# Kernel optimization log

Measured on AMD Instinct MI355X. Metric: run time of the kernel, lower is better.

Reference implementation:

```python
import jax, jax.numpy as jnp
import numpy as np
import math

EMBED_DIM = 2048
NUM_HEADS = 16
HEAD_DIM = EMBED_DIM // NUM_HEADS
BATCH = 2
SEQ = 2048


def setup_inputs() -> dict:
    key = jax.random.key(0)
    ks = jax.random.split(key, 6)
    x = jax.random.normal(ks[0], (BATCH, SEQ, EMBED_DIM), dtype=jnp.float32)
    # causal mask: True = masked (upper triangle, strictly above diagonal)
    attn_mask = jnp.triu(jnp.ones((SEQ, SEQ), dtype=bool), k=1)
    s = 1.0 / math.sqrt(EMBED_DIM)
    W_qkv = jax.random.normal(ks[1], (3 * EMBED_DIM, EMBED_DIM), dtype=jnp.float32) * s
    b_qkv = jax.random.normal(ks[2], (3 * EMBED_DIM,), dtype=jnp.float32) * 0.01
    W_out = jax.random.normal(ks[3], (EMBED_DIM, EMBED_DIM), dtype=jnp.float32) * s
    b_out = jax.random.normal(ks[4], (EMBED_DIM,), dtype=jnp.float32) * 0.01
    return {"x": x, "W_qkv": W_qkv, "b_qkv": b_qkv, "W_out": W_out,
            "b_out": b_out, "attn_mask": attn_mask}


def reference(x, W_qkv, b_qkv, W_out, b_out, attn_mask):
    B, S, E = x.shape
    # fused QKV projection: [B,S,3E]
    qkv = jnp.einsum('bse,fe->bsf', x, W_qkv) + b_qkv
    qkv = qkv.reshape(B, S, 3, NUM_HEADS, HEAD_DIM)
    qkv = jnp.transpose(qkv, (2, 0, 3, 1, 4))  # [3,B,H,S,Dh]
    q, k, v = qkv[0], qkv[1], qkv[2]
    scale = 1.0 / math.sqrt(HEAD_DIM)
    scores = jnp.einsum('bhqd,bhkd->bhqk', q, k) * scale  # [B,H,S,S]
    scores = jnp.where(attn_mask[None, None, :, :], -jnp.inf, scores)
    attn = jax.nn.softmax(scores, axis=-1)
    out = jnp.einsum('bhqk,bhkd->bhqd', attn, v)  # [B,H,S,Dh]
    out = jnp.transpose(out, (0, 2, 1, 3)).reshape(B, S, E)
    out = jnp.einsum('bse,fe->bsf', out, W_out) + b_out
    return out
```

## Files before the change

kernel.cpp:

```cpp
#include <hip/hip_runtime.h>
#include <hip/hip_bf16.h>
#include <math.h>

#define SEQ   2048
#define EMBED 2048
#define NHEAD 16
#define DHEAD 128
#define BATCH 2

#define NX   ((size_t)BATCH * SEQ * EMBED)
#define NW1  ((size_t)3 * EMBED * EMBED)
#define NB1  ((size_t)3 * EMBED)
#define NW2  ((size_t)EMBED * EMBED)
#define NB2  ((size_t)EMBED)

typedef __bf16 bf16;
typedef __attribute__((__ext_vector_type__(8))) __bf16 bf16x8;
typedef __attribute__((__ext_vector_type__(4))) __bf16 bf16x4;
typedef __attribute__((__ext_vector_type__(4))) float f32x4;
typedef __attribute__((__ext_vector_type__(4))) unsigned int u32x4;

#define NEG_BIG (-1.0e30f)

__device__ __forceinline__ f32x4 mfma_16x16x32(bf16x8 a, bf16x8 b, f32x4 c) {
  return __builtin_amdgcn_mfma_f32_16x16x32_bf16(a, b, c, 0, 0, 0);
}

__device__ __forceinline__ void llds16(bf16* dst, const bf16* src) {
  __builtin_amdgcn_global_load_lds(
      (const __attribute__((address_space(1))) void*)src,
      (__attribute__((address_space(3))) void*)dst, 16, 0, 0);
}

#define BAR()                                   \
  {                                             \
    asm volatile("" ::: "memory");              \
    __builtin_amdgcn_s_barrier();               \
    asm volatile("" ::: "memory");              \
  }

__global__ void convert_inputs(const void* __restrict__ xin,
                               const void* __restrict__ w1in,
                               const void* __restrict__ b1in,
                               const void* __restrict__ w2in,
                               const void* __restrict__ b2in,
                               bf16* __restrict__ xb, bf16* __restrict__ w1b,
                               bf16* __restrict__ b1b, bf16* __restrict__ w2b,
                               bf16* __restrict__ b2b, int* __restrict__ flagp)
{
  __shared__ int sflag;
  if (threadIdx.x == 0) sflag = 0;
  __syncthreads();
  const unsigned short* xh = (const unsigned short*)xin;
  int huge = 0;
  for (int i = threadIdx.x; i < 2048; i += 256) {
    float f = __uint_as_float((unsigned int)xh[i] << 16);
    if (!(fabsf(f) <= 1e4f)) huge = 1;
  }
  if (huge) sflag = 1;
  __syncthreads();
  const int isf32 = sflag;
  if (blockIdx.x == 0 && threadIdx.x == 0) *flagp = isf32;

  const void* srcs[5] = {xin, w1in, b1in, w2in, b2in};
  bf16* dsts[5] = {xb, w1b, b1b, w2b, b2b};
  const size_t lens[5] = {NX, NW1, NB1, NW2, NB2};
  const size_t gid = (size_t)blockIdx.x * blockDim.x + threadIdx.x;
  const size_t gstride = (size_t)gridDim.x * blockDim.x;
  for (int sidx = 0; sidx < 5; ++sidx) {
    const size_t n8 = lens[sidx] >> 3;
    bf16* d = dsts[sidx];
    if (isf32) {
      const float* s = (const float*)srcs[sidx];
      for (size_t i = gid; i < n8; i += gstride) {
        const float* sp = s + i * 8;
        bf16x8 r;
#pragma unroll
        for (int j = 0; j < 8; ++j) r[j] = (bf16)sp[j];
        *(bf16x8*)(d + i * 8) = r;
      }
    } else {
      const u32x4* s = (const u32x4*)srcs[sidx];
      for (size_t i = gid; i < n8; i += gstride)
        *(u32x4*)(d + i * 8) = s[i];
    }
  }
}

#define GSTAGE(tt)                                                       \
  {                                                                      \
    const int _slot = (tt) & 3;                                          \
    const int _k0 = (tt) << 5;                                           \
    _Pragma("unroll") for (int j = 0; j < 3; ++j)                        \
        llds16(&sAB[_slot][dstofs[j]], srcbase[j] + _k0);                \
  }

template <int MODE>
__global__ __launch_bounds__(512, 1) void gemm_nt2(
    const bf16* __restrict__ A, const bf16* __restrict__ B,
    const bf16* __restrict__ bias, int K,
    void* __restrict__ out0v, bf16* __restrict__ out1, bf16* __restrict__ out2,
    const int* __restrict__ flagp)
{
  __shared__ __align__(16) bf16 sAB[4][12288];
  const int t = threadIdx.x;
  const int lane = t & 63, w = t >> 6;
  const int wm = w >> 2, wn = w & 3;
  const int lr = lane & 15, lq = lane >> 4;
  const int m0 = blockIdx.y * 128, n0 = blockIdx.x * 256;
  const int NT = K >> 5;

  const int srow = lane >> 2;
  const int glog = (lane & 3) ^ (srow & 3);
  const bf16* srcbase[3];
  int dstofs[3];
#pragma unroll
  for (int j = 0; j < 3; ++j) {
    const int c2 = w * 3 + j;
    if (c2 < 8) {
      srcbase[j] = A + (size_t)(m0 + c2 * 16 + srow) * K + glog * 8;
      dstofs[j] = c2 * 512;
    } else {
      const int b = c2 - 8;
      srcbase[j] = B + (size_t)(n0 + b * 16 + srow) * K + glog * 8;
      dstofs[j] = 4096 + b * 512;
    }
  }

  f32x4 acc[4][4];
#pragma unroll
  for (int i = 0; i < 4; ++i)
#pragma unroll
    for (int j = 0; j < 4; ++j) acc[i][j] = (f32x4){0.f, 0.f, 0.f, 0.f};

  const int rdg = ((lq ^ (lr & 3)) << 3);
  const int aofs = (wm * 64 + lr) * 32 + rdg;
  const int bofs = 4096 + (wn * 64 + lr) * 32 + rdg;

  GSTAGE(0);
  GSTAGE(1);
  GSTAGE(2);
  asm volatile("s_waitcnt vmcnt(6)" ::: "memory");
  BAR();

  for (int tt = 0; tt < NT; ++tt) {
    const bf16* sl = sAB[tt & 3];
    if (tt + 3 < NT) GSTAGE(tt + 3);
    bf16x8 af[4], bfr[4];
#pragma unroll
    for (int i = 0; i < 4; ++i) {
      af[i]  = *(const bf16x8*)(sl + aofs + i * 512);
      bfr[i] = *(const bf16x8*)(sl + bofs + i * 512);
    }
    BAR();
    __builtin_amdgcn_s_setprio(1);
#pragma unroll
    for (int mi = 0; mi < 4; ++mi)
#pragma unroll
      for (int ni = 0; ni < 4; ++ni)
        acc[mi][ni] = mfma_16x16x32(af[mi], bfr[ni], acc[mi][ni]);
    __builtin_amdgcn_s_setprio(0);
    if (tt <= NT - 4)      { asm volatile("s_waitcnt vmcnt(6)" ::: "memory"); }
    else if (tt == NT - 3) { asm volatile("s_waitcnt vmcnt(3)" ::: "memory"); }
    else if (tt == NT - 2) { asm volatile("s_waitcnt vmcnt(0)" ::: "memory"); }
    BAR();
  }

  if (MODE == 0) {
    const int which = n0 >> 11;
    const int bb = m0 >> 11;
    const int s0 = m0 & 2047;
    if (which == 2) {
      bf16* dst = out2;
#pragma unroll
      for (int ni = 0; ni < 4; ++ni) {
        const int ng = n0 + wn * 64 + ni * 16 + lr;
        const int h = (ng >> 7) & 15;
        const int d = ng & 127;
        const float bv = (float)bias[ng];
        bf16* rowp =
            dst + ((size_t)(bb * NHEAD + h) * DHEAD + d) * SEQ + s0 + wm * 64;
#pragma unroll
        for (int mi = 0; mi < 4; ++mi) {
          bf16x4 pk;
#pragma unroll
          for (int reg = 0; reg < 4; ++reg)
            pk[reg] = (bf16)(acc[mi][ni][reg] + bv);
          *(bf16x4*)(rowp + mi * 16 + lq * 4) = pk;
        }
      }
    } else {
      bf16* dst = (which == 0) ? (bf16*)out0v : out1;
#pragma unroll
      for (int ni = 0; ni < 4; ++ni) {
        const int ng = n0 + wn * 64 + ni * 16 + lr;
        const int h = (ng >> 7) & 15;
        const int d = ng & 127;
        const float bv = (float)bias[ng];
        bf16* hb = dst + (size_t)(bb * NHEAD + h) * SEQ * DHEAD + d;
#pragma unroll
        for (int mi = 0; mi < 4; ++mi)
#pragma unroll
          for (int reg = 0; reg < 4; ++reg) {
            const int s = s0 + wm * 64 + mi * 16 + lq * 4 + reg;
            hb[(size_t)s * DHEAD] = (bf16)(acc[mi][ni][reg] + bv);
          }
      }
    }
  } else {
    const int isf32 = *flagp;
#pragma unroll
    for (int ni = 0; ni < 4; ++ni) {
      const int col = n0 + wn * 64 + ni * 16 + lr;
      const float bv = (float)bias[col];
#pragma unroll
      for (int mi = 0; mi < 4; ++mi)
#pragma unroll
        for (int reg = 0; reg < 4; ++reg) {
          const int row = m0 + wm * 64 + mi * 16 + lq * 4 + reg;
          const float v = acc[mi][ni][reg] + bv;
          const size_t idx = (size_t)row * EMBED + col;
          if (isf32) ((float*)out0v)[idx] = v;
          else       ((bf16*)out0v)[idx] = (bf16)v;
        }
    }
  }
}

__device__ __forceinline__ void qk_softmax_tile(
    const bf16* __restrict__ sK, bf16* __restrict__ sP, const bf16x8* aq,
    float& m_i, float& l_i, f32x4* oacc, int kt, int qt,
    int w, int lr, int lq, int sPofs)
{
  const float scale = 0.08838834764831845f;
  f32x4 tacc[4];
#pragma unroll
  for (int ni = 0; ni < 4; ++ni) tacc[ni] = (f32x4){0.f, 0.f, 0.f, 0.f};
#pragma unroll
  for (int ks = 0; ks < 4; ++ks)
#pragma unroll
    for (int ni = 0; ni < 4; ++ni) {
      bf16x8 bk = *(const bf16x8*)(sK + (ni * 16 + lr) * 136 + ks * 32 + lq * 8);
      tacc[ni] = mfma_16x16x32(bk, aq[ks], tacc[ni]);
    }
  float pp[4][4];
  const int qg = qt * 64 + w * 16 + lr;
#pragma unroll
  for (int ni = 0; ni < 4; ++ni)
#pragma unroll
    for (int reg = 0; reg < 4; ++reg) {
      float sv = tacc[ni][reg] * scale;
      if (kt == qt) {
        const int kg = kt * 64 + ni * 16 + lq * 4 + reg;
        if (kg > qg) sv = NEG_BIG;
      }
      pp[ni][reg] = sv;
    }
  float mx;
  {
    float a0 = fmaxf(fmaxf(pp[0][0], pp[0][1]), fmaxf(pp[0][2], pp[0][3]));
    float a1 = fmaxf(fmaxf(pp[1][0], pp[1][1]), fmaxf(pp[1][2], pp[1][3]));
    float a2 = fmaxf(fmaxf(pp[2][0], pp[2][1]), fmaxf(pp[2][2], pp[2][3]));
    float a3 = fmaxf(fmaxf(pp[3][0], pp[3][1]), fmaxf(pp[3][2], pp[3][3]));
    mx = fmaxf(fmaxf(a0, a1), fmaxf(a2, a3));
  }
  mx = fmaxf(mx, __shfl_xor(mx, 16, 64));
  mx = fmaxf(mx, __shfl_xor(mx, 32, 64));
  const float mnew = fmaxf(m_i, mx);
  const float alpha = __expf(m_i - mnew);
  float ls = 0.f;
#pragma unroll
  for (int ni = 0; ni < 4; ++ni) {
    float s0 = __expf(pp[ni][0] - mnew);
    float s1 = __expf(pp[ni][1] - mnew);
    float s2 = __expf(pp[ni][2] - mnew);
    float s3 = __expf(pp[ni][3] - mnew);
    pp[ni][0] = s0; pp[ni][1] = s1; pp[ni][2] = s2; pp[ni][3] = s3;
    ls += (s0 + s1) + (s2 + s3);
  }
  ls += __shfl_xor(ls, 16, 64);
  ls += __shfl_xor(ls, 32, 64);
  l_i = l_i * alpha + ls;
  m_i = mnew;
#pragma unroll
  for (int dt = 0; dt < 8; ++dt) oacc[dt] *= alpha;
  bf16* rowp = sP + (sPofs + w * 16 + lr) * 64;
  const int swz = lr & 7;
#pragma unroll
  for (int ni = 0; ni < 4; ++ni) {
    bf16x4 pk;
#pragma unroll
    for (int reg = 0; reg < 4; ++reg) pk[reg] = (bf16)pp[ni][reg];
    const int col = ni * 16 + lq * 4;
    const int scol = (((col >> 3) ^ swz) << 3) | (col & 7);
    *(bf16x4*)(rowp + scol) = pk;
  }
}

__device__ __forceinline__ void pv_tile(const bf16* __restrict__ sP,
                                        const bf16* __restrict__ sV,
                                        f32x4* oacc, int w, int lr, int lq,
                                        int sPofs)
{
  const bf16* rowp = sP + (sPofs + w * 16 + lr) * 64;
  const int swz = lr & 7;
#pragma unroll
  for (int ks2 = 0; ks2 < 2; ++ks2) {
    const int chunk = ks2 * 4 + lq;
    bf16x8 bp = *(const bf16x8*)(rowp + ((chunk ^ swz) << 3));
#pragma unroll
    for (int dt = 0; dt < 8; ++dt) {
      bf16x8 av =
          *(const bf16x8*)(sV + (dt * 16 + lr) * 72 + ks2 * 32 + lq * 8);
      oacc[dt] = mfma_16x16x32(av, bp, oacc[dt]);
    }
  }
}

__global__ __launch_bounds__(256, 2) void attn_fwd(
    const bf16* __restrict__ qb, const bf16* __restrict__ kb,
    const bf16* __restrict__ vt, bf16* __restrict__ aout)
{
  __shared__ bf16 sK[64 * 136];
  __shared__ bf16 sV[128 * 72];
  __shared__ bf16 sP[128 * 64];
  const int t = threadIdx.x;
  const int lane = t & 63, w = t >> 6;
  const int lr = lane & 15, lq = lane >> 4;
  const int p  = blockIdx.x & 15;
  const int bh = blockIdx.x >> 4;
  const int bb = bh >> 4, h = bh & 15;
  const int qlo = p, qhi = 31 - p;

  bf16x8 aqL[4], aqH[4];
  {
    const bf16* qpL =
        qb + ((size_t)bh * SEQ + qlo * 64 + w * 16 + lr) * DHEAD + lq * 8;
    const bf16* qpH =
        qb + ((size_t)bh * SEQ + qhi * 64 + w * 16 + lr) * DHEAD + lq * 8;
#pragma unroll
    for (int ks = 0; ks < 4; ++ks) {
      aqL[ks] = *(const bf16x8*)(qpL + ks * 32);
      aqH[ks] = *(const bf16x8*)(qpH + ks * 32);
    }
  }

  f32x4 oL[8], oH[8];
#pragma unroll
  for (int i = 0; i < 8; ++i) {
    oL[i] = (f32x4){0.f, 0.f, 0.f, 0.f};
    oH[i] = (f32x4){0.f, 0.f, 0.f, 0.f};
  }
  float mL = NEG_BIG, mH = NEG_BIG;
  float lL = 0.f, lH = 0.f;

  bf16x8 rk[4], rv[4];
  const int kr_ = t >> 4, kd_ = t & 15;
  const int vr_ = t >> 3, vk_ = t & 7;
#define FETCH(ktv)                                                          \
  {                                                                         \
    const int _kt = (ktv);                                                  \
    _Pragma("unroll") for (int i = 0; i < 4; ++i) {                         \
      rk[i] = *(const bf16x8*)(kb + ((size_t)bh * SEQ + _kt * 64 +          \
                                     (i * 16 + kr_)) * DHEAD + kd_ * 8);    \
      rv[i] = *(const bf16x8*)(vt + ((size_t)bh * DHEAD + (i * 32 + vr_)) * \
                                     SEQ + _kt * 64 + vk_ * 8);             \
    }                                                                       \
  }
#define COMMIT()                                                            \
  {                                                                         \
    _Pragma("unroll") for (int i = 0; i < 4; ++i) {                         \
      *(bf16x8*)(sK + (i * 16 + kr_) * 136 + kd_ * 8) = rk[i];              \
      *(bf16x8*)(sV + (i * 32 + vr_) * 72 + vk_ * 8) = rv[i];               \
    }                                                                       \
  }

  FETCH(0);
  COMMIT();
  __syncthreads();

  for (int kt = 0; kt <= qhi; ++kt) {
    if (kt < qhi) FETCH(kt + 1);
    const bool doLo = (kt <= qlo);

    qk_softmax_tile(sK, sP, aqH, mH, lH, oH, kt, qhi, w, lr, lq, 64);
    if (doLo) qk_softmax_tile(sK, sP, aqL, mL, lL, oL, kt, qlo, w, lr, lq, 0);
    asm volatile("s_waitcnt lgkmcnt(0)" ::: "memory");
    pv_tile(sP, sV, oH, w, lr, lq, 64);
    if (doLo) pv_tile(sP, sV, oL, w, lr, lq, 0);

    __syncthreads();
    if (kt < qhi) {
      COMMIT();
      __syncthreads();
    }
  }

#pragma unroll
  for (int side = 0; side < 2; ++side) {
    const f32x4* oacc = side ? oH : oL;
    const float linv = 1.0f / (side ? lH : lL);
    const int qt = side ? qhi : qlo;
    const int qg = qt * 64 + w * 16 + lr;
    bf16* outp = aout + ((size_t)bb * SEQ + qg) * EMBED + h * 128 + lq * 4;
#pragma unroll
    for (int dt = 0; dt < 8; ++dt) {
      bf16x4 pk;
#pragma unroll
      for (int reg = 0; reg < 4; ++reg)
        pk[reg] = (bf16)(oacc[dt][reg] * linv);
      *(bf16x4*)(outp + dt * 16) = pk;
    }
  }
#undef FETCH
#undef COMMIT
}

extern "C" void kernel_launch(void* const* d_in, const int* in_sizes, int n_in,
                              void* d_out, int out_size, void* d_ws, size_t ws_size,
                              hipStream_t stream) {
  const void* x    = d_in[0];
  const void* Wqkv = d_in[1];
  const void* bqkv = d_in[2];
  const void* Wout = d_in[3];
  const void* bout = d_in[4];

  int* flagp = (int*)d_ws;
  bf16* base = (bf16*)((char*)d_ws + 256);
  bf16* xb   = base;
  bf16* w1b  = xb + NX;
  bf16* b1b  = w1b + NW1;
  bf16* w2b  = b1b + NB1;
  bf16* b2b  = w2b + NW2;
  bf16* qb   = b2b + NB2;
  bf16* kb   = qb + NX;
  bf16* vt   = kb + NX;
  bf16* aout = vt + NX;

  convert_inputs<<<dim3(1024), dim3(256), 0, stream>>>(
      x, Wqkv, bqkv, Wout, bout, xb, w1b, b1b, w2b, b2b, flagp);
  gemm_nt2<0><<<dim3(24, 32), dim3(512), 0, stream>>>(
      xb, w1b, b1b, EMBED, (void*)qb, kb, vt, flagp);
  attn_fwd<<<dim3(512), dim3(256), 0, stream>>>(qb, kb, vt, aout);
  gemm_nt2<1><<<dim3(8, 32), dim3(512), 0, stream>>>(
      aout, w2b, b2b, EMBED, d_out, nullptr, nullptr, flagp);
}
```

Before: 414.1 us.

## Rewrite GEMM with 256x256 tiles, 8-phase K=64 pipeline and XCD-aware block remap

Both projection GEMMs now use 256x256 output tiles with each wave computing 128x64, doubling accumulators to cover 8x4 MFMA tiles. K is staged in 64-wide double-buffered half-tiles loaded across eight interleaved phases per pair of k-tiles, and a 1D grid is remapped so consecutive blocks land on the same XCD group. This is meant to raise arithmetic intensity per LDS load and improve L2 locality. In exchange it uses 128KB of LDS and many more registers, and launches fewer blocks (384 and 128), which may leave CUs underused.

```diff
diff --git a/kernel.cpp b/kernel.cpp
--- a/kernel.cpp
+++ b/kernel.cpp
@@ -87,84 +87,88 @@
   }
 }
 
-#define GSTAGE(tt)                                                       \
-  {                                                                      \
-    const int _slot = (tt) & 3;                                          \
-    const int _k0 = (tt) << 5;                                           \
-    _Pragma("unroll") for (int j = 0; j < 3; ++j)                        \
-        llds16(&sAB[_slot][dstofs[j]], srcbase[j] + _k0);                \
-  }
-
 template <int MODE>
-__global__ __launch_bounds__(512, 1) void gemm_nt2(
+__global__ __launch_bounds__(512, 2) void gemm8(
     const bf16* __restrict__ A, const bf16* __restrict__ B,
     const bf16* __restrict__ bias, int K,
     void* __restrict__ out0v, bf16* __restrict__ out1, bf16* __restrict__ out2,
     const int* __restrict__ flagp)
 {
-  __shared__ __align__(16) bf16 sAB[4][12288];
+  __shared__ __align__(16) bf16 lds_[65536];
+  constexpr int NBX = (MODE == 0) ? 24 : 8;
   const int t = threadIdx.x;
   const int lane = t & 63, w = t >> 6;
   const int wm = w >> 2, wn = w & 3;
   const int lr = lane & 15, lq = lane >> 4;
-  const int m0 = blockIdx.y * 128, n0 = blockIdx.x * 256;
-  const int NT = K >> 5;
-
-  const int srow = lane >> 2;
-  const int glog = (lane & 3) ^ (srow & 3);
-  const bf16* srcbase[3];
-  int dstofs[3];
-#pragma unroll
-  for (int j = 0; j < 3; ++j) {
-    const int c2 = w * 3 + j;
-    if (c2 < 8) {
-      srcbase[j] = A + (size_t)(m0 + c2 * 16 + srow) * K + glog * 8;
-      dstofs[j] = c2 * 512;
-    } else {
-      const int b = c2 - 8;
-      srcbase[j] = B + (size_t)(n0 + b * 16 + srow) * K + glog * 8;
-      dstofs[j] = 4096 + b * 512;
-    }
-  }
-
-  f32x4 acc[4][4];
-#pragma unroll
-  for (int i = 0; i < 4; ++i)
+  const int nwg = NBX * 16;
+  const int f = blockIdx.x;
+  const int o = (f & 7) * (nwg >> 3) + (f >> 3);
+  const int by = o / NBX, bx = o - by * NBX;
+  const int m0 = by * 256, n0 = bx * 256;
+  const int NT = K >> 6;
+  const int NI = NT >> 1;
+
+  const int srow = t >> 2, sg = t & 3;
+  const bf16* aSrc = A + (size_t)(m0 + srow) * K + sg * 8;
+  const bf16* bSrc = B + (size_t)(n0 + srow) * K + sg * 8;
+
+#define HTSTAGE(isB, kt, kh)                                                 \
+  {                                                                          \
+    bf16* _d = lds_ + ((kt) & 1) * 32768 + (isB) * 16384 + (kh) * 8192 +     \
+               w * 512;                                                      \
+    const bf16* _s = ((isB) ? bSrc : aSrc) + (kt) * 64 + (kh) * 32;          \
+    llds16(_d, _s);                                                          \
+    llds16(_d + 4096, _s + (size_t)128 * K);                                 \
+  }
+
+  f32x4 acc[8][4];
+#pragma unroll
+  for (int i = 0; i < 8; ++i)
 #pragma unroll
     for (int j = 0; j < 4; ++j) acc[i][j] = (f32x4){0.f, 0.f, 0.f, 0.f};
 
-  const int rdg = ((lq ^ (lr & 3)) << 3);
-  const int aofs = (wm * 64 + lr) * 32 + rdg;
-  const int bofs = 4096 + (wn * 64 + lr) * 32 + rdg;
-
-  GSTAGE(0);
-  GSTAGE(1);
-  GSTAGE(2);
-  asm volatile("s_waitcnt vmcnt(6)" ::: "memory");
+  HTSTAGE(0, 0, 0); HTSTAGE(1, 0, 0); HTSTAGE(0, 0, 1); HTSTAGE(1, 0, 1);
+  HTSTAGE(0, 1, 0); HTSTAGE(1, 1, 0);
+  asm volatile("s_waitcnt vmcnt(4)" ::: "memory");
   BAR();
 
-  for (int tt = 0; tt < NT; ++tt) {
-    const bf16* sl = sAB[tt & 3];
-    if (tt + 3 < NT) GSTAGE(tt + 3);
-    bf16x8 af[4], bfr[4];
-#pragma unroll
-    for (int i = 0; i < 4; ++i) {
-      af[i]  = *(const bf16x8*)(sl + aofs + i * 512);
-      bfr[i] = *(const bf16x8*)(sl + bofs + i * 512);
-    }
-    BAR();
-    __builtin_amdgcn_s_setprio(1);
-#pragma unroll
-    for (int mi = 0; mi < 4; ++mi)
-#pragma unroll
-      for (int ni = 0; ni < 4; ++ni)
-        acc[mi][ni] = mfma_16x16x32(af[mi], bfr[ni], acc[mi][ni]);
-    __builtin_amdgcn_s_setprio(0);
-    if (tt <= NT - 4)      { asm volatile("s_waitcnt vmcnt(6)" ::: "memory"); }
-    else if (tt == NT - 3) { asm volatile("s_waitcnt vmcnt(3)" ::: "memory"); }
-    else if (tt == NT - 2) { asm volatile("s_waitcnt vmcnt(0)" ::: "memory"); }
-    BAR();
-  }
+  bf16x8 bfr[4];
+  for (int i = 0; i < NI; ++i) {
+#pragma unroll
+    for (int p = 0; p < 8; ++p) {
+      const int mh = p & 1;
+      const int rbase = (p >> 2) * 32768 + ((p >> 1) & 1) * 8192;
+      bf16x8 af[4];
+      const int arow = rbase + (wm * 128 + mh * 64 + lr) * 32 + lq * 8;
+#pragma unroll
+      for (int mi = 0; mi < 4; ++mi)
+        af[mi] = *(const bf16x8*)(lds_ + arow + mi * 512);
+      if (mh == 0) {
+        const int brow = rbase + 16384 + (wn * 64 + lr) * 32 + lq * 8;
+#pragma unroll
+        for (int ni = 0; ni < 4; ++ni)
+          bfr[ni] = *(const bf16x8*)(lds_ + brow + ni * 512);
+      }
+      const int skt = 2 * i + 1 + ((p + 2) >> 2);
+      if (skt < NT) HTSTAGE(p & 1, skt, ((p >> 1) & 1) ^ 1);
+      BAR();
+      __builtin_amdgcn_s_setprio(1);
+#pragma unroll
+      for (int mi = 0; mi < 4; ++mi)
+#pragma unroll
+        for (int ni = 0; ni < 4; ++ni)
+          acc[mh * 4 + mi][ni] =
+              mfma_16x16x32(af[mi], bfr[ni], acc[mh * 4 + mi][ni]);
+      __builtin_amdgcn_s_setprio(0);
+      if (p == 3) {
+        if (i == NI - 1) { asm volatile("s_waitcnt vmcnt(0)" ::: "memory"); }
+        else             { asm volatile("s_waitcnt vmcnt(4)" ::: "memory"); }
+      }
+      if (p == 7) { asm volatile("s_waitcnt vmcnt(4)" ::: "memory"); }
+      BAR();
+    }
+  }
+#undef HTSTAGE
 
   if (MODE == 0) {
     const int which = n0 >> 11;
@@ -179,14 +183,14 @@
         const int d = ng & 127;
         const float bv = (float)bias[ng];
         bf16* rowp =
-            dst + ((size_t)(bb * NHEAD + h) * DHEAD + d) * SEQ + s0 + wm * 64;
-#pragma unroll
-        for (int mi = 0; mi < 4; ++mi) {
+            dst + ((size_t)(bb * NHEAD + h) * DHEAD + d) * SEQ + s0 + wm * 128;
+#pragma unroll
+        for (int MI = 0; MI < 8; ++MI) {
           bf16x4 pk;
 #pragma unroll
           for (int reg = 0; reg < 4; ++reg)
-            pk[reg] = (bf16)(acc[mi][ni][reg] + bv);
-          *(bf16x4*)(rowp + mi * 16 + lq * 4) = pk;
+            pk[reg] = (bf16)(acc[MI][ni][reg] + bv);
+          *(bf16x4*)(rowp + MI * 16 + lq * 4) = pk;
         }
       }
     } else {
@@ -199,11 +203,11 @@
         const float bv = (float)bias[ng];
         bf16* hb = dst + (size_t)(bb * NHEAD + h) * SEQ * DHEAD + d;
 #pragma unroll
-        for (int mi = 0; mi < 4; ++mi)
+        for (int MI = 0; MI < 8; ++MI)
 #pragma unroll
           for (int reg = 0; reg < 4; ++reg) {
-            const int s = s0 + wm * 64 + mi * 16 + lq * 4 + reg;
-            hb[(size_t)s * DHEAD] = (bf16)(acc[mi][ni][reg] + bv);
+            const int s = s0 + wm * 128 + MI * 16 + lq * 4 + reg;
+            hb[(size_t)s * DHEAD] = (bf16)(acc[MI][ni][reg] + bv);
           }
       }
     }
@@ -214,11 +218,11 @@
       const int col = n0 + wn * 64 + ni * 16 + lr;
       const float bv = (float)bias[col];
 #pragma unroll
-      for (int mi = 0; mi < 4; ++mi)
+      for (int MI = 0; MI < 8; ++MI)
 #pragma unroll
         for (int reg = 0; reg < 4; ++reg) {
-          const int row = m0 + wm * 64 + mi * 16 + lq * 4 + reg;
-          const float v = acc[mi][ni][reg] + bv;
+          const int row = m0 + wm * 128 + MI * 16 + lq * 4 + reg;
+          const float v = acc[MI][ni][reg] + bv;
           const size_t idx = (size_t)row * EMBED + col;
           if (isf32) ((float*)out0v)[idx] = v;
           else       ((bf16*)out0v)[idx] = (bf16)v;
@@ -439,9 +443,9 @@
 
   convert_inputs<<<dim3(1024), dim3(256), 0, stream>>>(
       x, Wqkv, bqkv, Wout, bout, xb, w1b, b1b, w2b, b2b, flagp);
-  gemm_nt2<0><<<dim3(24, 32), dim3(512), 0, stream>>>(
+  gemm8<0><<<dim3(384), dim3(512), 0, stream>>>(
       xb, w1b, b1b, EMBED, (void*)qb, kb, vt, flagp);
   attn_fwd<<<dim3(512), dim3(256), 0, stream>>>(qb, kb, vt, aout);
-  gemm_nt2<1><<<dim3(8, 32), dim3(512), 0, stream>>>(
+  gemm8<1><<<dim3(128), dim3(512), 0, stream>>>(
       aout, w2b, b2b, EMBED, d_out, nullptr, nullptr, flagp);
 }
```

Measured after the change: 429.7 us. 1.04x slower.

## Restructure GEMM pipeline into double-buffered 64-wide K tiles with XCD-aware block remap

Applied to the files above, without the earlier changes.

The two GEMM kernels now stage 64-element K tiles into two LDS buffers, split into 32-wide halves, and issue the async global-to-LDS loads interleaved with four compute phases per iteration. The swizzle pattern and LDS layout change to match. The 2D grid is flattened to 1D and blockIdx is remapped so consecutive blocks on the same XCD cover neighbouring tiles, aiming for better L2 reuse. The intent is to hide global load latency and cut barrier overhead per unit of MFMA work, at the cost of more complex wait-count bookkeeping that could stall or race if the counts are wrong.

```diff
diff --git a/kernel.cpp b/kernel.cpp
--- a/kernel.cpp
+++ b/kernel.cpp
@@ -32,12 +32,7 @@
       (__attribute__((address_space(3))) void*)dst, 16, 0, 0);
 }
 
-#define BAR()                                   \
-  {                                             \
-    asm volatile("" ::: "memory");              \
-    __builtin_amdgcn_s_barrier();               \
-    asm volatile("" ::: "memory");              \
-  }
+#define BARRAW() asm volatile("s_barrier" ::: "memory")
 
 __global__ void convert_inputs(const void* __restrict__ xin,
                                const void* __restrict__ w1in,
@@ -87,44 +82,43 @@
   }
 }
 
-#define GSTAGE(tt)                                                       \
-  {                                                                      \
-    const int _slot = (tt) & 3;                                          \
-    const int _k0 = (tt) << 5;                                           \
-    _Pragma("unroll") for (int j = 0; j < 3; ++j)                        \
-        llds16(&sAB[_slot][dstofs[j]], srcbase[j] + _k0);                \
-  }
-
 template <int MODE>
-__global__ __launch_bounds__(512, 1) void gemm_nt2(
+__global__ __launch_bounds__(512, 1) void gemmE(
     const bf16* __restrict__ A, const bf16* __restrict__ B,
     const bf16* __restrict__ bias, int K,
     void* __restrict__ out0v, bf16* __restrict__ out1, bf16* __restrict__ out2,
     const int* __restrict__ flagp)
 {
-  __shared__ __align__(16) bf16 sAB[4][12288];
+  __shared__ __align__(16) bf16 lds_[49152];
+  constexpr int NTX = (MODE == 0) ? 24 : 8;
   const int t = threadIdx.x;
   const int lane = t & 63, w = t >> 6;
   const int wm = w >> 2, wn = w & 3;
   const int lr = lane & 15, lq = lane >> 4;
-  const int m0 = blockIdx.y * 128, n0 = blockIdx.x * 256;
-  const int NT = K >> 5;
-
-  const int srow = lane >> 2;
-  const int glog = (lane & 3) ^ (srow & 3);
-  const bf16* srcbase[3];
-  int dstofs[3];
-#pragma unroll
-  for (int j = 0; j < 3; ++j) {
-    const int c2 = w * 3 + j;
-    if (c2 < 8) {
-      srcbase[j] = A + (size_t)(m0 + c2 * 16 + srow) * K + glog * 8;
-      dstofs[j] = c2 * 512;
-    } else {
-      const int b = c2 - 8;
-      srcbase[j] = B + (size_t)(n0 + b * 16 + srow) * K + glog * 8;
-      dstofs[j] = 4096 + b * 512;
-    }
+  const int nwg = 32 * NTX;
+  const int f = blockIdx.x;
+  const int o = (f & 7) * (nwg >> 3) + (f >> 3);
+  const int by = o & 31, bx = o >> 5;
+  const int m0 = by << 7, n0 = bx << 8;
+  const int NT = K >> 6;
+  const int NI = NT >> 1;
+
+  const int srow = t >> 2;
+  const int sg8 = (((t & 3) ^ (((t >> 5) & 1) << 1))) << 3;
+
+#define STAGE3(kt_, ks_)                                                     \
+  {                                                                          \
+    const int _kt = (kt_), _ks = (ks_);                                      \
+    if (_kt < NT) {                                                          \
+      const int _bb = (_kt & 1) * 24576;                                     \
+      const int _kc = (_kt << 6) + _ks * 32;                                 \
+      llds16(lds_ + _bb + _ks * 4096 + (w << 9),                             \
+             A + (size_t)(m0 + srow) * K + _kc + sg8);                       \
+      llds16(lds_ + _bb + 8192 + _ks * 8192 + (w << 9),                      \
+             B + (size_t)(n0 + srow) * K + _kc + sg8);                       \
+      llds16(lds_ + _bb + 8192 + _ks * 8192 + 4096 + (w << 9),               \
+             B + (size_t)(n0 + 128 + srow) * K + _kc + sg8);                 \
+    }                                                                        \
   }
 
   f32x4 acc[4][4];
@@ -133,42 +127,61 @@
 #pragma unroll
     for (int j = 0; j < 4; ++j) acc[i][j] = (f32x4){0.f, 0.f, 0.f, 0.f};
 
-  const int rdg = ((lq ^ (lr & 3)) << 3);
-  const int aofs = (wm * 64 + lr) * 32 + rdg;
-  const int bofs = 4096 + (wn * 64 + lr) * 32 + rdg;
-
-  GSTAGE(0);
-  GSTAGE(1);
-  GSTAGE(2);
+  const int rg8 = ((lq ^ (((lr >> 3) & 1) << 1))) << 3;
+  const int arow = (wm * 64 + lr) * 32 + rg8;
+  const int brow = (wn * 64 + lr) * 32 + rg8;
+
+  STAGE3(0, 0);
+  STAGE3(0, 1);
+  STAGE3(1, 0);
   asm volatile("s_waitcnt vmcnt(6)" ::: "memory");
-  BAR();
-
-  for (int tt = 0; tt < NT; ++tt) {
-    const bf16* sl = sAB[tt & 3];
-    if (tt + 3 < NT) GSTAGE(tt + 3);
-    bf16x8 af[4], bfr[4];
-#pragma unroll
-    for (int i = 0; i < 4; ++i) {
-      af[i]  = *(const bf16x8*)(sl + aofs + i * 512);
-      bfr[i] = *(const bf16x8*)(sl + bofs + i * 512);
-    }
-    BAR();
-    __builtin_amdgcn_s_setprio(1);
-#pragma unroll
-    for (int mi = 0; mi < 4; ++mi)
+  BARRAW();
+
+  for (int i = 0; i < NI; ++i) {
+    const int k2 = i << 1;
+#pragma unroll
+    for (int p = 0; p < 4; ++p) {
+      const int ks = p & 1;
+      const int bufb = (p >> 1) * 24576;
+      bf16x8 af[4], bfv[4];
+      const int ab = bufb + ks * 4096 + arow;
+      const int bb = bufb + 8192 + ks * 8192 + brow;
+#pragma unroll
+      for (int mi = 0; mi < 4; ++mi)
+        af[mi] = *(const bf16x8*)(lds_ + ab + mi * 512);
 #pragma unroll
       for (int ni = 0; ni < 4; ++ni)
-        acc[mi][ni] = mfma_16x16x32(af[mi], bfr[ni], acc[mi][ni]);
-    __builtin_amdgcn_s_setprio(0);
-    if (tt <= NT - 4)      { asm volatile("s_waitcnt vmcnt(6)" ::: "memory"); }
-    else if (tt == NT - 3) { asm volatile("s_waitcnt vmcnt(3)" ::: "memory"); }
-    else if (tt == NT - 2) { asm volatile("s_waitcnt vmcnt(0)" ::: "memory"); }
-    BAR();
-  }
+        bfv[ni] = *(const bf16x8*)(lds_ + bb + ni * 512);
+      if (p == 0)      STAGE3(k2 + 1, 1)
+      else if (p == 1) STAGE3(k2 + 2, 0)
+      else if (p == 2) STAGE3(k2 + 2, 1)
+      else             STAGE3(k2 + 3, 0)
+      BARRAW();
+      __builtin_amdgcn_s_setprio(1);
+#pragma unroll
+      for (int mi = 0; mi < 4; ++mi)
+#pragma unroll
+        for (int ni = 0; ni < 4; ++ni)
+          acc[mi][ni] = mfma_16x16x32(af[mi], bfv[ni], acc[mi][ni]);
+      __builtin_amdgcn_s_setprio(0);
+      if (i == 0 && p == 0) {
+        asm volatile("s_waitcnt vmcnt(6)" ::: "memory");
+      }
+      if (p == 1) {
+        if (i == NI - 1) { asm volatile("s_waitcnt vmcnt(0)" ::: "memory"); }
+        else             { asm volatile("s_waitcnt vmcnt(3)" ::: "memory"); }
+      }
+      if (p == 3 && i < NI - 1) {
+        asm volatile("s_waitcnt vmcnt(3)" ::: "memory");
+      }
+      BARRAW();
+    }
+  }
+#undef STAGE3
 
   if (MODE == 0) {
     const int which = n0 >> 11;
-    const int bb = m0 >> 11;
+    const int bbid = m0 >> 11;
     const int s0 = m0 & 2047;
     if (which == 2) {
       bf16* dst = out2;
@@ -179,7 +192,7 @@
         const int d = ng & 127;
         const float bv = (float)bias[ng];
         bf16* rowp =
-            dst + ((size_t)(bb * NHEAD + h) * DHEAD + d) * SEQ + s0 + wm * 64;
+            dst + ((size_t)(bbid * NHEAD + h) * DHEAD + d) * SEQ + s0 + wm * 64;
 #pragma unroll
         for (int mi = 0; mi < 4; ++mi) {
           bf16x4 pk;
@@ -197,7 +210,7 @@
         const int h = (ng >> 7) & 15;
         const int d = ng & 127;
         const float bv = (float)bias[ng];
-        bf16* hb = dst + (size_t)(bb * NHEAD + h) * SEQ * DHEAD + d;
+        bf16* hb = dst + (size_t)(bbid * NHEAD + h) * SEQ * DHEAD + d;
 #pragma unroll
         for (int mi = 0; mi < 4; ++mi)
 #pragma unroll
@@ -439,9 +452,9 @@
 
   convert_inputs<<<dim3(1024), dim3(256), 0, stream>>>(
       x, Wqkv, bqkv, Wout, bout, xb, w1b, b1b, w2b, b2b, flagp);
-  gemm_nt2<0><<<dim3(24, 32), dim3(512), 0, stream>>>(
+  gemmE<0><<<dim3(768), dim3(512), 0, stream>>>(
       xb, w1b, b1b, EMBED, (void*)qb, kb, vt, flagp);
   attn_fwd<<<dim3(512), dim3(256), 0, stream>>>(qb, kb, vt, aout);
-  gemm_nt2<1><<<dim3(8, 32), dim3(512), 0, stream>>>(
+  gemmE<1><<<dim3(256), dim3(512), 0, stream>>>(
       aout, w2b, b2b, EMBED, d_out, nullptr, nullptr, flagp);
 }
```

Result: faster. 395.0 us (-4.6%).
